# Performance work log

Measured on AMD Instinct MI355X. Metric: run time of the kernel, lower is better.

## Reference

```python
import jax, jax.numpy as jnp
import numpy as np

_SCAN_CHUNK = 32


def _causal_decay_scan(x, decay, init):
    """Inclusive scan out[t] = decay*out[t-1] + x[t], chunked closed form.
    x: [B,H,T,D], decay: [1,H,1], init: [B,H,D]. Returns [B,H,T,D]."""
    B, H, T, D = x.shape
    C = min(_SCAN_CHUNK, T)
    assert T % C == 0
    nC = T // C
    log_decay = jnp.log(jnp.clip(decay.astype(jnp.float32), 1e-8, None))  # [1,H,1]
    c_idx = jnp.arange(C, dtype=jnp.float32)
    log_p = log_decay[..., None] * c_idx.reshape(1, 1, C, 1)              # [1,H,C,1]
    p = jnp.exp(log_p)
    inv_p = jnp.exp(-log_p)
    init_p = jnp.exp(log_decay[..., None] * (c_idx + 1.0).reshape(1, 1, C, 1))
    # [nC, B, H, C, D] so lax.scan chains chunk states causally
    xc = x.reshape(B, H, nC, C, D).transpose(2, 0, 1, 3, 4).astype(jnp.float32)

    def step(state, chunk):  # state [B,H,D], chunk [B,H,C,D]
        cs = jnp.cumsum(chunk * inv_p, axis=2)
        out = cs * p + state[:, :, None, :] * init_p
        return out[:, :, -1, :], out

    _, outs = jax.lax.scan(step, init.astype(jnp.float32), xc)
    return outs.transpose(1, 2, 0, 3, 4).reshape(B, H, T, D).astype(x.dtype)


def _phi(x):
    return jax.nn.elu(x) + 1.0


def setup_inputs() -> dict:
    key = jax.random.key(0)
    ks = jax.random.split(key, 5)
    B, T, hidden, H = 4, 4096, 1024, 16
    s = 1.0 / np.sqrt(hidden)
    x = jax.random.normal(ks[0], (B, T, hidden), dtype=jnp.float32)
    Wqkv = jax.random.normal(ks[1], (3 * hidden, hidden), dtype=jnp.float32) * s
    Wout = jax.random.normal(ks[2], (hidden, hidden), dtype=jnp.float32) * s
    Wgate = jax.random.normal(ks[3], (hidden, hidden), dtype=jnp.float32) * s
    bgate = jnp.zeros((hidden,), dtype=jnp.float32)
    logit = float(np.log(0.95 / 0.05))  # sigmoid(logit) == 0.95
    decay_param = jnp.full((H,), logit, dtype=jnp.float32)
    return {"x": x, "Wqkv": Wqkv, "Wout": Wout, "Wgate": Wgate,
            "bgate": bgate, "decay_param": decay_param}


def reference(x, Wqkv, Wout, Wgate, bgate, decay_param):
    B, T, hidden = x.shape
    H = decay_param.shape[0]
    D = hidden // H
    qkv = x @ Wqkv.T                       # [B,T,3*hidden]
    q, k, v = jnp.split(qkv, 3, axis=-1)
    # [B,T,hidden] -> [B,H,T,D]
    q = q.reshape(B, T, H, D).transpose(0, 2, 1, 3)
    k = k.reshape(B, T, H, D).transpose(0, 2, 1, 3)
    v = v.reshape(B, T, H, D).transpose(0, 2, 1, 3)
    q = _phi(q)
    k = _phi(k)
    decay = jax.nn.sigmoid(decay_param).reshape(1, H, 1)
    kv_init = jnp.zeros((B, H, D), dtype=x.dtype)
    ksum_init = jnp.zeros((B, H, D), dtype=x.dtype)
    running_kv = _causal_decay_scan(k * v, decay, kv_init)
    running_ksum = _causal_decay_scan(k, decay, ksum_init)
    den = jnp.clip(jnp.sum(q * running_ksum, axis=-1, keepdims=True), 1e-6, None)
    out = q * running_kv / den             # [B,H,T,D]
    v_direct = v.transpose(0, 2, 1, 3).reshape(B, T, hidden)
    out = out.transpose(0, 2, 1, 3).reshape(B, T, hidden)
    g = jax.nn.sigmoid(out @ Wgate.T + bgate)
    out = g * out + (1.0 - g) * v_direct
    return out @ Wout.T
```

## Files before the change

### kernel.cpp

```cpp
#include <hip/hip_runtime.h>

typedef unsigned short u16;
typedef __bf16 bf16x8 __attribute__((ext_vector_type(8)));
typedef float f32x4 __attribute__((ext_vector_type(4)));

#define BB 4
#define TT 4096
#define HID 1024
#define NH 16
#define HD 64
#define BT (BB*TT)
#define NCH 128
#define LOG_NCH 7
#define CLEN (TT/NCH)

__device__ __forceinline__ float bf2f(u16 u) {
    return __uint_as_float(((unsigned)u) << 16);
}
__device__ __forceinline__ u16 f2bf(float f) {
    unsigned u = __float_as_uint(f);
    unsigned r = 0x7FFFu + ((u >> 16) & 1u);
    return (u16)((u + r) >> 16);
}
__device__ __forceinline__ float phi(float x) {
    return x > 0.f ? x + 1.f : __expf(x);
}
__device__ __forceinline__ float sigmoidf(float x) {
    return 1.f / (1.f + __expf(-x));
}
__device__ __forceinline__ float4 u4_to_f4(ushort4 u) {
    return make_float4(bf2f(u.x), bf2f(u.y), bf2f(u.z), bf2f(u.w));
}

#define CN1 (BT*HID/4)
#define CN2 (3*HID*HID/4)
#define CN3 (HID*HID/4)
#define CN4 (HID*HID/4)
__global__ void convert_all(const float4* __restrict__ x,    const float4* __restrict__ wqkv,
                            const float4* __restrict__ wgate, const float4* __restrict__ wout,
                            ushort4* __restrict__ xb,    ushort4* __restrict__ wqkvb,
                            ushort4* __restrict__ wgateb, ushort4* __restrict__ woutb) {
    int i = blockIdx.x * 256 + threadIdx.x;
    const float4* src; ushort4* dst; int j;
    if (i < CN1)                 { src = x;     dst = xb;     j = i; }
    else if (i < CN1+CN2)        { src = wqkv;  dst = wqkvb;  j = i - CN1; }
    else if (i < CN1+CN2+CN3)    { src = wgate; dst = wgateb; j = i - CN1 - CN2; }
    else                         { src = wout;  dst = woutb;  j = i - CN1 - CN2 - CN3; }
    float4 f = src[j];
    ushort4 u;
    u.x = f2bf(f.x); u.y = f2bf(f.y); u.z = f2bf(f.z); u.w = f2bf(f.w);
    dst[j] = u;
}

template<int EPI>
__global__ __launch_bounds__(512, 2)
void gemm256(const u16* __restrict__ A, const u16* __restrict__ Bm,
             int M, int N, int K, void* __restrict__ Cout,
             const float* __restrict__ bg,
             const u16* __restrict__ attn,
             const u16* __restrict__ qkv)
{
    __shared__ u16 As[2][256 * 64];
    __shared__ u16 Bs[2][256 * 64];
    const int tid  = threadIdx.x;
    const int wave = tid >> 6;
    const int lane = tid & 63;
    const int r16  = lane & 15;
    const int m0 = blockIdx.y * 256;
    const int n0 = blockIdx.x * 256;
    const int wm = (wave & 1) * 128;
    const int wn = (wave >> 1) * 64;

    f32x4 acc[8][4];
    #pragma unroll
    for (int i = 0; i < 8; ++i)
        #pragma unroll
        for (int j = 0; j < 4; ++j)
            acc[i][j] = (f32x4){0.f, 0.f, 0.f, 0.f};

    bf16x8 af[4][2];
    bf16x8 bq[2][2];

    auto STAGE_A = [&](int k0, int buf, int mq) {
        #pragma unroll
        for (int l = 0; l < 2; ++l) {
            int q    = wave * 2 + l;
            int row0 = (q >> 3) * 128 + mq * 64 + (q & 7) * 8;
            int row  = row0 + (lane >> 3);
            int lc   = (lane & 7) ^ (row & 7);
            const u16* g = A + (size_t)(m0 + row) * K + k0 + lc * 8;
            __builtin_amdgcn_global_load_lds(
                (const __attribute__((address_space(1))) void*)g,
                (__attribute__((address_space(3))) void*)&As[buf][row0 * 64], 16, 0, 0);
        }
    };
    auto STAGE_B = [&](int k0, int buf, int nq) {
        #pragma unroll
        for (int l = 0; l < 2; ++l) {
            int q    = wave * 2 + l;
            int row0 = (q >> 2) * 64 + nq * 32 + (q & 3) * 8;
            int row  = row0 + (lane >> 3);
            int lc   = (lane & 7) ^ (row & 7);
            const u16* g = Bm + (size_t)(n0 + row) * K + k0 + lc * 8;
            __builtin_amdgcn_global_load_lds(
                (const __attribute__((address_space(1))) void*)g,
                (__attribute__((address_space(3))) void*)&Bs[buf][row0 * 64], 16, 0, 0);
        }
    };

#define DS_A(BUF, MQ)                                                          \
    _Pragma("unroll") for (int i_ = 0; i_ < 4; ++i_)                           \
    _Pragma("unroll") for (int ks_ = 0; ks_ < 2; ++ks_) {                      \
        int pcq = (ks_ * 4 + (lane >> 4)) ^ (r16 & 7);                         \
        af[i_][ks_] = *(const bf16x8*)                                         \
            &As[BUF][(wm + (MQ) * 64 + i_ * 16 + r16) * 64 + pcq * 8];         \
    }
#define DS_B(BUF, NQ)                                                          \
    _Pragma("unroll") for (int j_ = 0; j_ < 2; ++j_)                           \
    _Pragma("unroll") for (int ks_ = 0; ks_ < 2; ++ks_) {                      \
        int pcq = (ks_ * 4 + (lane >> 4)) ^ (r16 & 7);                         \
        bq[j_][ks_] = *(const bf16x8*)                                         \
            &Bs[BUF][(wn + (NQ) * 32 + j_ * 16 + r16) * 64 + pcq * 8];         \
    }
#define MFMA_Q(MQ, NQ)                                                         \
    __builtin_amdgcn_s_setprio(1);                                             \
    _Pragma("unroll") for (int i_ = 0; i_ < 4; ++i_)                           \
    _Pragma("unroll") for (int j_ = 0; j_ < 2; ++j_)                           \
    _Pragma("unroll") for (int ks_ = 0; ks_ < 2; ++ks_)                        \
        acc[(MQ) * 4 + i_][(NQ) * 2 + j_] =                                    \
            __builtin_amdgcn_mfma_f32_16x16x32_bf16(                           \
                af[i_][ks_], bq[j_][ks_], acc[(MQ) * 4 + i_][(NQ) * 2 + j_],   \
                0, 0, 0);                                                      \
    __builtin_amdgcn_s_setprio(0);
#define SB __builtin_amdgcn_sched_barrier(0)
#define PH_MID  SB; __builtin_amdgcn_s_barrier();                              \
                asm volatile("s_waitcnt lgkmcnt(0)" ::: "memory"); SB;
#define PH_END  SB; __builtin_amdgcn_s_barrier(); SB;
#define PH_END_VM(N)  SB; asm volatile("s_waitcnt vmcnt(" #N ")" ::: "memory");\
                __builtin_amdgcn_s_barrier(); SB;

    const int niter = K >> 7;

    STAGE_A(0, 0, 0); STAGE_B(0, 0, 0); STAGE_A(0, 0, 1); STAGE_B(0, 0, 1);
    STAGE_B(64, 1, 0); STAGE_A(64, 1, 1);
    PH_END_VM(4);

    for (int i = 0; i < niter - 1; ++i) {
        const int kb = i * 128;
        DS_A(0, 0) DS_B(0, 0)
        STAGE_A(kb + 64, 1, 0);
        PH_MID; MFMA_Q(0, 0); PH_END;
        DS_A(0, 1)
        STAGE_B(kb + 64, 1, 1);
        PH_MID; MFMA_Q(1, 0); PH_END;
        DS_B(0, 1)
        STAGE_B(kb + 128, 0, 0);
        PH_MID; MFMA_Q(1, 1); PH_END;
        DS_A(0, 0)
        STAGE_A(kb + 128, 0, 1);
        PH_MID; MFMA_Q(0, 1); PH_END_VM(4);
        DS_A(1, 0) DS_B(1, 0)
        STAGE_A(kb + 128, 0, 0);
        PH_MID; MFMA_Q(0, 0); PH_END;
        DS_A(1, 1)
        STAGE_B(kb + 128, 0, 1);
        PH_MID; MFMA_Q(1, 0); PH_END;
        DS_B(1, 1)
        STAGE_B(kb + 192, 1, 0);
        PH_MID; MFMA_Q(1, 1); PH_END;
        DS_A(1, 0)
        STAGE_A(kb + 192, 1, 1);
        PH_MID; MFMA_Q(0, 1); PH_END_VM(4);
    }

    {
        const int kb = (niter - 1) * 128;
        DS_A(0, 0) DS_B(0, 0)
        STAGE_A(kb + 64, 1, 0);
        PH_MID; MFMA_Q(0, 0); PH_END;
        DS_A(0, 1)
        STAGE_B(kb + 64, 1, 1);
        PH_MID; MFMA_Q(1, 0); PH_END;
        DS_B(0, 1)
        PH_MID; MFMA_Q(1, 1); PH_END;
        DS_A(0, 0)
        PH_MID; MFMA_Q(0, 1); PH_END_VM(0);
        DS_A(1, 0) DS_B(1, 0)
        PH_MID; MFMA_Q(0, 0); PH_END;
        DS_A(1, 1)
        PH_MID; MFMA_Q(1, 0); PH_END;
        DS_B(1, 1)
        PH_MID; MFMA_Q(1, 1); PH_END;
        DS_A(1, 0)
        PH_MID; MFMA_Q(0, 1); PH_END;
    }

    #pragma unroll
    for (int mi = 0; mi < 8; ++mi) {
        int rowb = m0 + wm + mi * 16 + (lane >> 4) * 4;
        #pragma unroll
        for (int nj = 0; nj < 4; ++nj) {
            int col = n0 + wn + nj * 16 + r16;
            #pragma unroll
            for (int r = 0; r < 4; ++r) {
                float v = acc[mi][nj][r];
                size_t row = (size_t)(rowb + r);
                if (EPI == 0) {
                    ((u16*)Cout)[row * N + col] = f2bf(v);
                } else if (EPI == 1) {
                    float g  = sigmoidf(v + bg[col]);
                    float at = bf2f(attn[row * HID + col]);
                    float vd = bf2f(qkv[row * (3 * HID) + 2 * HID + col]);
                    ((u16*)Cout)[row * HID + col] = f2bf(g * at + (1.f - g) * vd);
                } else {
                    ((float*)Cout)[row * N + col] = v;
                }
            }
        }
    }
#undef DS_A
#undef DS_B
#undef MFMA_Q
#undef SB
#undef PH_MID
#undef PH_END
#undef PH_END_VM
}

__global__ void scan_finals(const u16* __restrict__ qkv, const float* __restrict__ decay_param,
                            float* __restrict__ ckv, float* __restrict__ cks) {
    int g  = blockIdx.x * 16 + (threadIdx.x >> 4);
    int sl = threadIdx.x & 15;
    int c = g & (NCH - 1);
    int h = (g >> LOG_NCH) & (NH - 1);
    int b = g >> (LOG_NCH + 4);
    float decay = sigmoidf(decay_param[h]);
    const u16* kp = qkv + (size_t)(b * TT + c * CLEN) * (3 * HID) + HID + h * HD + sl * 4;
    float4 skv = make_float4(0.f, 0.f, 0.f, 0.f);
    float4 sks = make_float4(0.f, 0.f, 0.f, 0.f);
    for (int t = 0; t < CLEN; ++t) {
        float4 k = u4_to_f4(*(const ushort4*)kp);
        float4 v = u4_to_f4(*(const ushort4*)(kp + HID));
        k.x = phi(k.x); k.y = phi(k.y); k.z = phi(k.z); k.w = phi(k.w);
        skv.x = decay * skv.x + k.x * v.x;  skv.y = decay * skv.y + k.y * v.y;
        skv.z = decay * skv.z + k.z * v.z;  skv.w = decay * skv.w + k.w * v.w;
        sks.x = decay * sks.x + k.x;        sks.y = decay * sks.y + k.y;
        sks.z = decay * sks.z + k.z;        sks.w = decay * sks.w + k.w;
        kp += 3 * HID;
    }
    *(float4*)(ckv + (size_t)g * 64 + sl * 4) = skv;
    *(float4*)(cks + (size_t)g * 64 + sl * 4) = sks;
}

__global__ void scan_prefix(float* __restrict__ ckv, float* __restrict__ cks,
                            const float* __restrict__ decay_param) {
    int bh = blockIdx.x;
    int h  = bh & (NH - 1);
    int lane = threadIdx.x;
    float decay = sigmoidf(decay_param[h]);
    float dC = powf(decay, (float)CLEN);
    float* pkv = ckv + (size_t)bh * NCH * 64 + lane;
    float* pks = cks + (size_t)bh * NCH * 64 + lane;
    float fkv = 0.f, fks = 0.f;
    for (int c = 0; c < NCH; ++c) {
        float lkv = pkv[c * 64], lks = pks[c * 64];
        pkv[c * 64] = fkv; pks[c * 64] = fks;
        fkv = fkv * dC + lkv;
        fks = fks * dC + lks;
    }
}

__global__ void scan_apply(const u16* __restrict__ qkv, const float* __restrict__ decay_param,
                           const float* __restrict__ ckv, const float* __restrict__ cks,
                           u16* __restrict__ attn) {
    int g  = blockIdx.x * 16 + (threadIdx.x >> 4);
    int sl = threadIdx.x & 15;
    int c = g & (NCH - 1);
    int h = (g >> LOG_NCH) & (NH - 1);
    int b = g >> (LOG_NCH + 4);
    float decay = sigmoidf(decay_param[h]);
    float4 skv = *(const float4*)(ckv + (size_t)g * 64 + sl * 4);
    float4 sks = *(const float4*)(cks + (size_t)g * 64 + sl * 4);
    const u16* qp = qkv + (size_t)(b * TT + c * CLEN) * (3 * HID) + h * HD + sl * 4;
    u16* op = attn + (size_t)(b * TT + c * CLEN) * HID + h * HD + sl * 4;
    for (int t = 0; t < CLEN; ++t) {
        float4 q = u4_to_f4(*(const ushort4*)qp);
        float4 k = u4_to_f4(*(const ushort4*)(qp + HID));
        float4 v = u4_to_f4(*(const ushort4*)(qp + 2 * HID));
        q.x = phi(q.x); q.y = phi(q.y); q.z = phi(q.z); q.w = phi(q.w);
        k.x = phi(k.x); k.y = phi(k.y); k.z = phi(k.z); k.w = phi(k.w);
        skv.x = decay * skv.x + k.x * v.x;  skv.y = decay * skv.y + k.y * v.y;
        skv.z = decay * skv.z + k.z * v.z;  skv.w = decay * skv.w + k.w * v.w;
        sks.x = decay * sks.x + k.x;        sks.y = decay * sks.y + k.y;
        sks.z = decay * sks.z + k.z;        sks.w = decay * sks.w + k.w;
        float s = q.x * sks.x + q.y * sks.y + q.z * sks.z + q.w * sks.w;
        s += __shfl_xor(s, 8);
        s += __shfl_xor(s, 4);
        s += __shfl_xor(s, 2);
        s += __shfl_xor(s, 1);
        float inv = 1.f / fmaxf(s, 1e-6f);
        ushort4 o;
        o.x = f2bf(q.x * skv.x * inv); o.y = f2bf(q.y * skv.y * inv);
        o.z = f2bf(q.z * skv.z * inv); o.w = f2bf(q.w * skv.w * inv);
        *(ushort4*)op = o;
        qp += 3 * HID;
        op += HID;
    }
}

extern "C" void kernel_launch(void* const* d_in, const int* in_sizes, int n_in,
                              void* d_out, int out_size, void* d_ws, size_t ws_size,
                              hipStream_t stream) {
    const float* x     = (const float*)d_in[0];
    const float* Wqkv  = (const float*)d_in[1];
    const float* Wout  = (const float*)d_in[2];
    const float* Wgate = (const float*)d_in[3];
    const float* bgate = (const float*)d_in[4];
    const float* decay = (const float*)d_in[5];

    u16* xb     = (u16*)d_ws;
    u16* wqkvb  = xb    + (size_t)BT * HID;
    u16* wgateb = wqkvb + (size_t)3 * HID * HID;
    u16* woutb  = wgateb + (size_t)HID * HID;
    u16* qkvb   = woutb + (size_t)HID * HID;
    u16* out2b  = qkvb  + (size_t)BT * 3 * HID;
    float* ckv  = (float*)(out2b + (size_t)BT * HID);
    float* cks  = ckv + (size_t)BB * NH * NCH * HD;
    u16* attnb  = xb;

    convert_all<<<(CN1 + CN2 + CN3 + CN4) / 256, 256, 0, stream>>>(
        (const float4*)x, (const float4*)Wqkv, (const float4*)Wgate, (const float4*)Wout,
        (ushort4*)xb, (ushort4*)wqkvb, (ushort4*)wgateb, (ushort4*)woutb);

    gemm256<0><<<dim3(3 * HID / 256, BT / 256), 512, 0, stream>>>(
        xb, wqkvb, BT, 3 * HID, HID, qkvb, nullptr, nullptr, nullptr);

    scan_finals<<<BB * NH * NCH / 16, 256, 0, stream>>>(qkvb, decay, ckv, cks);
    scan_prefix<<<BB * NH, 64, 0, stream>>>(ckv, cks, decay);
    scan_apply<<<BB * NH * NCH / 16, 256, 0, stream>>>(qkvb, decay, ckv, cks, attnb);

    gemm256<1><<<dim3(HID / 256, BT / 256), 512, 0, stream>>>(
        attnb, wgateb, BT, HID, HID, out2b, bgate, attnb, qkvb);

    gemm256<2><<<dim3(HID / 256, BT / 256), 512, 0, stream>>>(
        out2b, woutb, BT, HID, HID, d_out, nullptr, nullptr, nullptr);
}
```

Baseline: 387.0 us.

## Double-buffer GEMM fragment registers and relax LDS/VMEM waits in pipeline

Splits the A and B fragment registers into two sets each (afX/afY, bqA/bqB), so LDS reads for the next quadrant can be issued while MFMAs on the current quadrant run. The quadrant order is changed so that fragments are reused across adjacent MFMA phases, which cuts redundant LDS reads. Global-to-LDS staging is reordered, and the waitcnt thresholds (lgkmcnt/vmcnt) are tuned to keep more loads in flight. This adds register pressure from the extra fragment buffers, and the hand-tuned counters could let data be read before it arrives.

```diff
diff --git a/kernel.cpp b/kernel.cpp
--- a/kernel.cpp
+++ b/kernel.cpp
@@ -78,8 +78,8 @@
         for (int j = 0; j < 4; ++j)
             acc[i][j] = (f32x4){0.f, 0.f, 0.f, 0.f};
 
-    bf16x8 af[4][2];
-    bf16x8 bq[2][2];
+    bf16x8 afX[4][2], afY[4][2];
+    bf16x8 bqA[2][2], bqB[2][2];
 
     auto STAGE_A = [&](int k0, int buf, int mq) {
         #pragma unroll
@@ -108,91 +108,85 @@
         }
     };
 
-#define DS_A(BUF, MQ)                                                          \
+#define RD_A(BUF, MQ, DST)                                                     \
     _Pragma("unroll") for (int i_ = 0; i_ < 4; ++i_)                           \
     _Pragma("unroll") for (int ks_ = 0; ks_ < 2; ++ks_) {                      \
         int pcq = (ks_ * 4 + (lane >> 4)) ^ (r16 & 7);                         \
-        af[i_][ks_] = *(const bf16x8*)                                         \
+        DST[i_][ks_] = *(const bf16x8*)                                        \
             &As[BUF][(wm + (MQ) * 64 + i_ * 16 + r16) * 64 + pcq * 8];         \
     }
-#define DS_B(BUF, NQ)                                                          \
+#define RD_B(BUF, NQ, DST)                                                     \
     _Pragma("unroll") for (int j_ = 0; j_ < 2; ++j_)                           \
     _Pragma("unroll") for (int ks_ = 0; ks_ < 2; ++ks_) {                      \
         int pcq = (ks_ * 4 + (lane >> 4)) ^ (r16 & 7);                         \
-        bq[j_][ks_] = *(const bf16x8*)                                         \
+        DST[j_][ks_] = *(const bf16x8*)                                        \
             &Bs[BUF][(wn + (NQ) * 32 + j_ * 16 + r16) * 64 + pcq * 8];         \
     }
-#define MFMA_Q(MQ, NQ)                                                         \
+#define MFMA_Q(MQ, NQ, AF, BQ)                                                 \
     __builtin_amdgcn_s_setprio(1);                                             \
     _Pragma("unroll") for (int i_ = 0; i_ < 4; ++i_)                           \
     _Pragma("unroll") for (int j_ = 0; j_ < 2; ++j_)                           \
     _Pragma("unroll") for (int ks_ = 0; ks_ < 2; ++ks_)                        \
         acc[(MQ) * 4 + i_][(NQ) * 2 + j_] =                                    \
             __builtin_amdgcn_mfma_f32_16x16x32_bf16(                           \
-                af[i_][ks_], bq[j_][ks_], acc[(MQ) * 4 + i_][(NQ) * 2 + j_],   \
-                0, 0, 0);                                                      \
+                AF[i_][ks_], BQ[j_][ks_],                                      \
+                acc[(MQ) * 4 + i_][(NQ) * 2 + j_], 0, 0, 0);                   \
     __builtin_amdgcn_s_setprio(0);
 #define SB __builtin_amdgcn_sched_barrier(0)
-#define PH_MID  SB; __builtin_amdgcn_s_barrier();                              \
-                asm volatile("s_waitcnt lgkmcnt(0)" ::: "memory"); SB;
-#define PH_END  SB; __builtin_amdgcn_s_barrier(); SB;
-#define PH_END_VM(N)  SB; asm volatile("s_waitcnt vmcnt(" #N ")" ::: "memory");\
-                __builtin_amdgcn_s_barrier(); SB;
+#define MID(NLG)  SB; __builtin_amdgcn_s_barrier();                            \
+    asm volatile("s_waitcnt lgkmcnt(" #NLG ")" ::: "memory"); SB;
+#define ENDV(NVM) SB; asm volatile("s_waitcnt vmcnt(" #NVM ")" ::: "memory");  \
+    __builtin_amdgcn_s_barrier(); SB;
 
     const int niter = K >> 7;
 
-    STAGE_A(0, 0, 0); STAGE_B(0, 0, 0); STAGE_A(0, 0, 1); STAGE_B(0, 0, 1);
-    STAGE_B(64, 1, 0); STAGE_A(64, 1, 1);
-    PH_END_VM(4);
+    STAGE_A(0, 0, 0);
+    STAGE_B(0, 0, 0);
+    STAGE_B(0, 0, 1);
+    STAGE_A(0, 0, 1);
+    STAGE_A(64, 1, 0);
+    STAGE_B(64, 1, 0);
+    STAGE_B(64, 1, 1);
+    SB; asm volatile("s_waitcnt vmcnt(10)" ::: "memory");
+    __builtin_amdgcn_s_barrier(); SB;
+    RD_A(0, 0, afX); RD_B(0, 0, bqA);
+    ENDV(8);
 
     for (int i = 0; i < niter - 1; ++i) {
         const int kb = i * 128;
-        DS_A(0, 0) DS_B(0, 0)
-        STAGE_A(kb + 64, 1, 0);
-        PH_MID; MFMA_Q(0, 0); PH_END;
-        DS_A(0, 1)
-        STAGE_B(kb + 64, 1, 1);
-        PH_MID; MFMA_Q(1, 0); PH_END;
-        DS_B(0, 1)
+        RD_B(0, 1, bqB);  STAGE_A(kb + 64, 1, 1);
+        MID(4);  MFMA_Q(0, 0, afX, bqA);  ENDV(8);
+        RD_A(0, 1, afY);  STAGE_A(kb + 128, 0, 0);
+        MID(8);  MFMA_Q(0, 1, afX, bqB);  ENDV(8);
         STAGE_B(kb + 128, 0, 0);
-        PH_MID; MFMA_Q(1, 1); PH_END;
-        DS_A(0, 0)
-        STAGE_A(kb + 128, 0, 1);
-        PH_MID; MFMA_Q(0, 1); PH_END_VM(4);
-        DS_A(1, 0) DS_B(1, 0)
-        STAGE_A(kb + 128, 0, 0);
-        PH_MID; MFMA_Q(0, 0); PH_END;
-        DS_A(1, 1)
-        STAGE_B(kb + 128, 0, 1);
-        PH_MID; MFMA_Q(1, 0); PH_END;
-        DS_B(1, 1)
+        MID(0);  MFMA_Q(1, 0, afY, bqA);  ENDV(8);
+        RD_A(1, 0, afX);  RD_B(1, 0, bqA);  STAGE_B(kb + 128, 0, 1);
+        MID(12); MFMA_Q(1, 1, afY, bqB);  ENDV(8);
+        RD_B(1, 1, bqB);  STAGE_A(kb + 128, 0, 1);
+        MID(4);  MFMA_Q(0, 0, afX, bqA);  ENDV(8);
+        RD_A(1, 1, afY);  STAGE_A(kb + 192, 1, 0);
+        MID(8);  MFMA_Q(0, 1, afX, bqB);  ENDV(8);
         STAGE_B(kb + 192, 1, 0);
-        PH_MID; MFMA_Q(1, 1); PH_END;
-        DS_A(1, 0)
-        STAGE_A(kb + 192, 1, 1);
-        PH_MID; MFMA_Q(0, 1); PH_END_VM(4);
+        MID(0);  MFMA_Q(1, 0, afY, bqA);  ENDV(8);
+        RD_A(0, 0, afX);  RD_B(0, 0, bqA);  STAGE_B(kb + 192, 1, 1);
+        MID(12); MFMA_Q(1, 1, afY, bqB);  ENDV(8);
     }
 
     {
         const int kb = (niter - 1) * 128;
-        DS_A(0, 0) DS_B(0, 0)
-        STAGE_A(kb + 64, 1, 0);
-        PH_MID; MFMA_Q(0, 0); PH_END;
-        DS_A(0, 1)
-        STAGE_B(kb + 64, 1, 1);
-        PH_MID; MFMA_Q(1, 0); PH_END;
-        DS_B(0, 1)
-        PH_MID; MFMA_Q(1, 1); PH_END;
-        DS_A(0, 0)
-        PH_MID; MFMA_Q(0, 1); PH_END_VM(0);
-        DS_A(1, 0) DS_B(1, 0)
-        PH_MID; MFMA_Q(0, 0); PH_END;
-        DS_A(1, 1)
-        PH_MID; MFMA_Q(1, 0); PH_END;
-        DS_B(1, 1)
-        PH_MID; MFMA_Q(1, 1); PH_END;
-        DS_A(1, 0)
-        PH_MID; MFMA_Q(0, 1); PH_END;
+        RD_B(0, 1, bqB);  STAGE_A(kb + 64, 1, 1);
+        MID(4);  MFMA_Q(0, 0, afX, bqA);  ENDV(8);
+        RD_A(0, 1, afY);
+        MID(8);  MFMA_Q(0, 1, afX, bqB);  ENDV(8);
+        MID(0);  MFMA_Q(1, 0, afY, bqA);  ENDV(4);
+        RD_A(1, 0, afX);  RD_B(1, 0, bqA);
+        MID(12); MFMA_Q(1, 1, afY, bqB);  ENDV(2);
+        RD_B(1, 1, bqB);
+        MID(4);  MFMA_Q(0, 0, afX, bqA);  ENDV(0);
+        RD_A(1, 1, afY);
+        MID(8);  MFMA_Q(0, 1, afX, bqB);  ENDV(0);
+        MID(0);  MFMA_Q(1, 0, afY, bqA);  ENDV(0);
+        MID(0);  MFMA_Q(1, 1, afY, bqB);
     }
 
     #pragma unroll
@@ -218,13 +212,12 @@
             }
         }
     }
-#undef DS_A
-#undef DS_B
+#undef RD_A
+#undef RD_B
 #undef MFMA_Q
 #undef SB
-#undef PH_MID
-#undef PH_END
-#undef PH_END_VM
+#undef MID
+#undef ENDV
 }
 
 __global__ void scan_finals(const u16* __restrict__ qkv, const float* __restrict__ decay_param,
```

After: 579.4 us. 1.5x slower.
